# Kernel tuning notes

Hardware: AMD Instinct MI355X
Metric: run time of the kernel (lower is better)

## Reference

```python
import jax, jax.numpy as jnp
import numpy as np

N_STEPS = 8


def _step(state, qop, dz_sub, W1, b1, W2, b2, W3, b3, W4, b4):
    # state [B,4], qop [B,1], dz_sub [B,1] -> residual-updated state [B,4]
    inp = jnp.concatenate([state, qop, dz_sub], axis=-1)  # [B,6]
    h = jax.nn.silu(inp @ W1 + b1)
    h = jax.nn.silu(h @ W2 + b2)
    h = jax.nn.silu(h @ W3 + b3)
    return state + (h @ W4 + b4)


def setup_inputs() -> dict:
    key = jax.random.key(0)
    ks = jax.random.split(key, 8)
    B = 262144
    H = 256
    # scale weights like xavier-ish init so activations stay sane
    def w(k, shape):
        fan_in = shape[0]
        return jax.random.normal(k, shape, dtype=jnp.float32) * (1.0 / np.sqrt(fan_in))
    state_dz = jax.random.normal(ks[0], (B, 6), dtype=jnp.float32)
    z_frac = jax.random.uniform(ks[1], (B,), dtype=jnp.float32)
    return {
        "state_dz": state_dz,
        "z_frac": z_frac,
        "W1": w(ks[2], (6, H)), "b1": jnp.zeros((H,), jnp.float32),
        "W2": w(ks[3], (H, H)), "b2": jnp.zeros((H,), jnp.float32),
        "W3": w(ks[4], (H, H)), "b3": jnp.zeros((H,), jnp.float32),
        "W4": w(ks[5], (H, 4)) * 0.1, "b4": jnp.zeros((4,), jnp.float32),
    }


def reference(state_dz, z_frac, W1, b1, W2, b2, W3, b3, W4, b4):
    # Faithful translation of CompositionalPINN.forward with z_frac of shape [B].
    # Torch uses max_steps = n_full.max().item() (host sync); running all N_STEPS
    # with the per-sample mask (n_full > step) yields identical math, since the
    # mask is 0 for step >= n_full.
    state = state_dz[:, :4]
    qop = state_dz[:, 4:5]
    dz_total = state_dz[:, 5:6]
    dz_sub = dz_total / N_STEPS

    continuous_steps = z_frac * N_STEPS            # [B]
    n_full = jnp.floor(continuous_steps)           # [B], kept float (compared vs step)
    frac_partial = continuous_steps - n_full       # [B]

    for step in range(N_STEPS):
        mask = (n_full > step).astype(state.dtype)[:, None]  # [B,1]
        new_state = _step(state, qop, dz_sub, W1, b1, W2, b2, W3, b3, W4, b4)
        state = mask * new_state + (1.0 - mask) * state

    dz_partial = frac_partial[:, None] * dz_sub
    has_partial = (frac_partial > 1e-6).astype(state.dtype)[:, None]
    partial_state = _step(state, qop, dz_partial, W1, b1, W2, b2, W3, b3, W4, b4)
    state = has_partial * partial_state + (1.0 - has_partial) * state
    return state
```

## Files before the change

kernel.cpp:

```cpp
#include <hip/hip_runtime.h>

typedef unsigned short u16;
typedef unsigned int u32;
typedef __attribute__((ext_vector_type(8))) short v8s;
typedef __attribute__((ext_vector_type(4))) float f32x4;

#define RPB 64
#define THREADS 256
#define NSB 512
#define W1F 0
#define W2F 8192
#define W3F 73728
#define W4F 139264
#define TOTW 143360
#define BH_OFF 286720
#define PERM_OFF 305152

#define MFMA(w, b, c) __builtin_amdgcn_mfma_f32_16x16x32_bf16((w), (b), (c), 0, 0, 0)

typedef __attribute__((address_space(1))) const unsigned int gu32;
typedef __attribute__((address_space(3))) unsigned int su32;
__device__ __forceinline__ void gld16(const u16* g, u16* l) {
  __builtin_amdgcn_global_load_lds((gu32*)g, (su32*)l, 16, 0, 0);
}

__device__ __forceinline__ u32 pk2(float a, float b) {
  u32 r;
  asm("v_cvt_pk_bf16_f32 %0, %1, %2" : "=v"(r) : "v"(a), "v"(b));
  return r;
}
__device__ __forceinline__ float bfu(u32 w, int hi) {
  return __uint_as_float(hi ? (w & 0xffff0000u) : (w << 16));
}
__device__ __forceinline__ f32x4 silu4(f32x4 v) {
  f32x4 r;
#pragma unroll
  for (int i = 0; i < 4; ++i) r[i] = v[i] * __builtin_amdgcn_rcpf(1.0f + __expf(-v[i]));
  return r;
}

__global__ void prep_weights(const float* __restrict__ W1, const float* __restrict__ b1,
                             const float* __restrict__ W2, const float* __restrict__ W3,
                             const float* __restrict__ W4, u16* __restrict__ Wf) {
  int e = blockIdx.x * 256 + threadIdx.x;
  if (e >= TOTW) return;
  float val = 0.0f;
  if (e < W2F) {
    int mt = e >> 9, idx = e & 511, l = idx >> 3, j = idx & 7;
    int q = l >> 4, m = l & 15;
    int f = 16 * (j >> 2) + 4 * q + (j & 3);
    int col = mt * 16 + m;
    val = (f < 6) ? W1[f * 256 + col]
        : ((f < 12) ? W1[(f - 6) * 256 + col]
        : ((f == 12) ? b1[col] : 0.0f));
  } else if (e < W3F) {
    int e2 = e - W2F, blk = e2 >> 9, idx = e2 & 511, l = idx >> 3, j = idx & 7;
    int ks = blk >> 4, mt = blk & 15, q = l >> 4, m = l & 15;
    int f = 32 * ks + 16 * (j >> 2) + 4 * q + (j & 3);
    val = W2[f * 256 + mt * 16 + m];
  } else if (e < W4F) {
    int e2 = e - W3F, blk = e2 >> 9, idx = e2 & 511, l = idx >> 3, j = idx & 7;
    int ks = blk >> 4, mt = blk & 15, q = l >> 4, m = l & 15;
    int f = 32 * ks + 16 * (j >> 2) + 4 * q + (j & 3);
    val = W3[f * 256 + mt * 16 + m];
  } else {
    int e2 = e - W4F, ks = e2 >> 9, idx = e2 & 511, l = idx >> 3, j = idx & 7;
    int q = l >> 4, m = l & 15;
    int f = 32 * ks + 16 * (j >> 2) + 4 * q + (j & 3);
    val = (m < 4) ? W4[f * 4 + m] : 0.0f;
  }
  Wf[e] = (u16)pk2(val, val);
}

__global__ void hist_blocks(const float* __restrict__ zf, int* __restrict__ bh, int B) {
  __shared__ int h[9];
  int t = threadIdx.x;
  if (t < 9) h[t] = 0;
  __syncthreads();
  int r = blockIdx.x * 512 + t;
  if (r < B) {
    int nf = min(max((int)floorf(zf[r] * 8.0f), 0), 8);
    atomicAdd(&h[nf], 1);
  }
  __syncthreads();
  if (t < 9) bh[blockIdx.x * 9 + t] = h[t];
}

__global__ void scan_offsets(int* __restrict__ bh) {
  __shared__ int S[NSB * 9];
  __shared__ int tot[9], ebase[9];
  int t = threadIdx.x;
  for (int i = t; i < NSB * 9; i += 512) S[i] = bh[i];
  __syncthreads();
  if (t < 9) {
    int s = 0;
    for (int b = 0; b < NSB; ++b) s += S[b * 9 + t];
    tot[t] = s;
  }
  __syncthreads();
  if (t == 0) {
    int s = 0;
    for (int i = 0; i < 9; ++i) { ebase[i] = s; s += tot[i]; }
  }
  __syncthreads();
  if (t < 9) {
    int off = ebase[t];
    for (int b = 0; b < NSB; ++b) { int c = S[b * 9 + t]; S[b * 9 + t] = off; off += c; }
  }
  __syncthreads();
  for (int i = t; i < NSB * 9; i += 512) bh[i] = S[i];
}

__global__ void scatter_sorted(const float* __restrict__ zf, const int* __restrict__ bh,
                               int* __restrict__ perm, int B) {
  __shared__ int off[9];
  int t = threadIdx.x;
  if (t < 9) off[t] = bh[blockIdx.x * 9 + t];
  __syncthreads();
  int r = blockIdx.x * 512 + t;
  if (r < B) {
    int nf = min(max((int)floorf(zf[r] * 8.0f), 0), 8);
    int pos = atomicAdd(&off[nf], 1);
    perm[pos] = r;
  }
}

__global__ __attribute__((amdgpu_flat_work_group_size(256, 256)))
__attribute__((amdgpu_waves_per_eu(2, 2))) void pinn_main(
    const float* __restrict__ sdz, const float* __restrict__ zf,
    const u16* __restrict__ Wf, const int* __restrict__ perm,
    const float* __restrict__ b2, const float* __restrict__ b3,
    const float* __restrict__ b4, float* __restrict__ out) {
  __shared__ __align__(16) u16 ringS[3][8192];
  __shared__ __align__(16) u16 W1s[8192];
  __shared__ __align__(16) u16 W4s[4096];
  __shared__ __align__(16) float biasS[528];
  __shared__ __align__(16) float stS[RPB * 4];
  __shared__ float qopS[RPB], dzS[RPB], fracS[RPB];
  __shared__ int nfS[RPB], rowG[RPB];

  const int t = threadIdx.x;
  const int lane = t & 63;
  const int q = lane >> 4;
  const int n = lane & 15;
  const int wv = t >> 6;
  const int rb = wv * 16;

  if (t < RPB) {
    int rg = perm[blockIdx.x * RPB + t];
    rowG[t] = rg;
    const float* p = sdz + (size_t)rg * 6;
    stS[t * 4 + 0] = p[0]; stS[t * 4 + 1] = p[1];
    stS[t * 4 + 2] = p[2]; stS[t * 4 + 3] = p[3];
    qopS[t] = p[4];
    dzS[t] = p[5] * 0.125f;
    float cs = zf[rg] * 8.0f;
    float nfl = floorf(cs);
    nfS[t] = (int)nfl;
    fracS[t] = cs - nfl;
  }
  biasS[t] = b2[t]; biasS[256 + t] = b3[t];
  if (t < 16) biasS[512 + t] = (t < 4) ? b4[t] : 0.0f;
#pragma unroll
  for (int c = 0; c < 4; ++c)
    gld16(Wf + W1F + (c * 4 + wv) * 512 + lane * 8, &W1s[(c * 4 + wv) * 512]);
#pragma unroll
  for (int c = 0; c < 2; ++c)
    gld16(Wf + W4F + (c * 4 + wv) * 512 + lane * 8, &W4s[(c * 4 + wv) * 512]);
  __syncthreads();
  const int maxnf = nfS[RPB - 1];

  f32x4 acc[16];
  v8s bact[8];
  const f32x4 Z4 = {0.0f, 0.0f, 0.0f, 0.0f};

#define ISSUE_SLICE(AP, BUF)                                                  \
  do {                                                                        \
    int sp_ = (AP) & 15;                                                      \
    int off_ = ((sp_ >> 3) ? W3F : W2F) + (sp_ & 7) * 8192;                   \
    u16* dst_ = &ringS[(BUF)][0];                                             \
    _Pragma("unroll") for (int c_ = 0; c_ < 4; ++c_)                          \
      gld16(Wf + off_ + (c_ * 4 + wv) * 512 + lane * 8,                       \
            dst_ + (c_ * 4 + wv) * 512);                                      \
  } while (0)

  int ap = 0;
  int bc = 0;
  ISSUE_SLICE(0, 0);

#define PACK_BACT()                                              \
  do {                                                           \
    _Pragma("unroll") for (int ks = 0; ks < 8; ++ks) {           \
      f32x4 a0 = silu4(acc[2 * ks]);                             \
      f32x4 a1 = silu4(acc[2 * ks + 1]);                         \
      union { int4 i; v8s s; } u_;                               \
      u_.i.x = (int)pk2(a0[0], a0[1]);                           \
      u_.i.y = (int)pk2(a0[2], a0[3]);                           \
      u_.i.z = (int)pk2(a1[0], a1[1]);                           \
      u_.i.w = (int)pk2(a1[2], a1[3]);                           \
      bact[ks] = u_.s;                                           \
    }                                                            \
  } while (0)

  for (int ev = 0; ev <= maxnf; ++ev) {
    const bool partial = (ev == maxnf);

    v8s b1f;
    {
      const int row = rb + n;
      const float4 st = *(const float4*)&stS[row * 4];
      const float qop = qopS[row];
      const float dzv = partial ? fracS[row] * dzS[row] : dzS[row];
      u32 h01 = pk2(st.x, st.y), h23 = pk2(st.z, st.w), hqd = pk2(qop, dzv);
      float l0 = st.x - bfu(h01, 0), l1 = st.y - bfu(h01, 1);
      float l2 = st.z - bfu(h23, 0), l3 = st.w - bfu(h23, 1);
      float lq = qop - bfu(hqd, 0), ld = dzv - bfu(hqd, 1);
      u32 w0 = 0, w1 = 0;
      if (q == 0) { w0 = h01; w1 = h23; }
      else if (q == 1) { w0 = hqd; w1 = pk2(l0, l1); }
      else if (q == 2) { w0 = pk2(l2, l3); w1 = pk2(lq, ld); }
      else { w0 = 0x00003F80u; }
      union { int4 i; v8s s; } u_;
      u_.i.x = (int)w0; u_.i.y = (int)w1; u_.i.z = 0; u_.i.w = 0;
      b1f = u_.s;
    }

#pragma unroll
    for (int mt = 0; mt < 16; ++mt) {
      const v8s w = *(const v8s*)&W1s[mt * 512 + lane * 8];
      acc[mt] = MFMA(w, b1f, Z4);
    }
    PACK_BACT();

#pragma unroll
    for (int layer = 0; layer < 2; ++layer) {
      const int Lb = (layer == 0) ? 0 : 256;
#pragma unroll
      for (int mt = 0; mt < 16; ++mt) {
        const float4 bb = *(const float4*)&biasS[Lb + mt * 16 + q * 4];
        const f32x4 binit = {bb.x, bb.y, bb.z, bb.w};
        acc[mt] = binit;
      }
#pragma unroll
      for (int ks = 0; ks < 8; ++ks) {
        int bn = bc + 1; if (bn == 3) bn = 0;
        ISSUE_SLICE(ap + 1, bn);
        asm volatile("s_waitcnt vmcnt(4)" ::: "memory");
        __builtin_amdgcn_sched_barrier(0);
        __builtin_amdgcn_s_barrier();
        __builtin_amdgcn_sched_barrier(0);
        asm volatile("" ::: "memory");
        const u16* buf = &ringS[bc][0];
        __builtin_amdgcn_s_setprio(1);
#pragma unroll
        for (int i = 0; i < 8; ++i) {
          const v8s w = *(const v8s*)&buf[i * 512 + lane * 8];
          acc[i] = MFMA(w, bact[ks], acc[i]);
        }
        __builtin_amdgcn_sched_barrier(0);
#pragma unroll
        for (int i = 8; i < 16; ++i) {
          const v8s w = *(const v8s*)&buf[i * 512 + lane * 8];
          acc[i] = MFMA(w, bact[ks], acc[i]);
        }
        __builtin_amdgcn_s_setprio(0);
        bc = bn; ++ap;
      }
      PACK_BACT();
    }

    {
      const float4 bb = *(const float4*)&biasS[512 + q * 4];
      f32x4 a4 = {bb.x, bb.y, bb.z, bb.w};
#pragma unroll
      for (int ks = 0; ks < 8; ++ks) {
        const v8s w = *(const v8s*)&W4s[ks * 512 + lane * 8];
        a4 = MFMA(w, bact[ks], a4);
      }
      if (q == 0) {
        const int row = rb + n;
        const bool act = partial ? (fracS[row] > 1e-6f) : (nfS[row] > ev);
        if (act) {
          float4 cur = *(float4*)&stS[row * 4];
          cur.x += a4[0]; cur.y += a4[1];
          cur.z += a4[2]; cur.w += a4[3];
          *(float4*)&stS[row * 4] = cur;
        }
      }
    }
  }
  __syncthreads();

  {
    const int i = t;
    out[(size_t)rowG[i >> 2] * 4 + (i & 3)] = stS[i];
  }
}

extern "C" void kernel_launch(void* const* d_in, const int* in_sizes, int n_in,
                              void* d_out, int out_size, void* d_ws, size_t ws_size,
                              hipStream_t stream) {
  const float* sdz = (const float*)d_in[0];
  const float* zfr = (const float*)d_in[1];
  const float* W1 = (const float*)d_in[2];
  const float* b1 = (const float*)d_in[3];
  const float* W2 = (const float*)d_in[4];
  const float* b2 = (const float*)d_in[5];
  const float* W3 = (const float*)d_in[6];
  const float* b3 = (const float*)d_in[7];
  const float* W4 = (const float*)d_in[8];
  const float* b4 = (const float*)d_in[9];

  char* ws = (char*)d_ws;
  u16* Wf = (u16*)ws;
  int* bh = (int*)(ws + BH_OFF);
  int* perm = (int*)(ws + PERM_OFF);

  const int B = in_sizes[1];

  prep_weights<<<(TOTW + 255) / 256, 256, 0, stream>>>(W1, b1, W2, W3, W4, Wf);
  hist_blocks<<<NSB, 512, 0, stream>>>(zfr, bh, B);
  scan_offsets<<<1, 512, 0, stream>>>(bh);
  scatter_sorted<<<NSB, 512, 0, stream>>>(zfr, bh, perm, B);
  pinn_main<<<B / RPB, THREADS, 0, stream>>>(sdz, zfr, Wf, perm, b2, b3, b4,
                                             (float*)d_out);
}
```

Before: 526.6 us.

## Stream W1 and W4 through the LDS ring to cut shared memory, raise occupancy

Drops the dedicated W1 and W4 shared-memory buffers and streams those weights through the existing triple-buffered ring alongside the W2/W3 slices. Each evaluation becomes one continuous W1→W2→W3→W4 pipeline. Per-row metadata is also compacted: nf and has_partial go into one u16, dz*frac is precomputed, and rowG is re-read from perm at the end. Less LDS per block plus waves_per_eu raised to 3 lets more blocks fit per CU. The cost is extra barriers and global reloads of W1/W4 on every step, with possible register pressure at the higher occupancy target.

```diff
diff --git a/kernel.cpp b/kernel.cpp
--- a/kernel.cpp
+++ b/kernel.cpp
@@ -126,18 +126,16 @@
 }
 
 __global__ __attribute__((amdgpu_flat_work_group_size(256, 256)))
-__attribute__((amdgpu_waves_per_eu(2, 2))) void pinn_main(
+__attribute__((amdgpu_waves_per_eu(2, 3))) void pinn_main(
     const float* __restrict__ sdz, const float* __restrict__ zf,
     const u16* __restrict__ Wf, const int* __restrict__ perm,
     const float* __restrict__ b2, const float* __restrict__ b3,
     const float* __restrict__ b4, float* __restrict__ out) {
   __shared__ __align__(16) u16 ringS[3][8192];
-  __shared__ __align__(16) u16 W1s[8192];
-  __shared__ __align__(16) u16 W4s[4096];
   __shared__ __align__(16) float biasS[528];
   __shared__ __align__(16) float stS[RPB * 4];
-  __shared__ float qopS[RPB], dzS[RPB], fracS[RPB];
-  __shared__ int nfS[RPB], rowG[RPB];
+  __shared__ float qopS[RPB], dzS[RPB], dzpS[RPB];
+  __shared__ u16 nfS[RPB];
 
   const int t = threadIdx.x;
   const int lane = t & 63;
@@ -148,45 +146,57 @@
 
   if (t < RPB) {
     int rg = perm[blockIdx.x * RPB + t];
-    rowG[t] = rg;
     const float* p = sdz + (size_t)rg * 6;
     stS[t * 4 + 0] = p[0]; stS[t * 4 + 1] = p[1];
     stS[t * 4 + 2] = p[2]; stS[t * 4 + 3] = p[3];
     qopS[t] = p[4];
-    dzS[t] = p[5] * 0.125f;
+    float dzsub = p[5] * 0.125f;
+    dzS[t] = dzsub;
     float cs = zf[rg] * 8.0f;
     float nfl = floorf(cs);
-    nfS[t] = (int)nfl;
-    fracS[t] = cs - nfl;
+    float fr = cs - nfl;
+    dzpS[t] = fr * dzsub;
+    nfS[t] = (u16)((int)nfl | ((fr > 1e-6f) ? 256 : 0));
   }
   biasS[t] = b2[t]; biasS[256 + t] = b3[t];
   if (t < 16) biasS[512 + t] = (t < 4) ? b4[t] : 0.0f;
-#pragma unroll
-  for (int c = 0; c < 4; ++c)
-    gld16(Wf + W1F + (c * 4 + wv) * 512 + lane * 8, &W1s[(c * 4 + wv) * 512]);
-#pragma unroll
-  for (int c = 0; c < 2; ++c)
-    gld16(Wf + W4F + (c * 4 + wv) * 512 + lane * 8, &W4s[(c * 4 + wv) * 512]);
-  __syncthreads();
-  const int maxnf = nfS[RPB - 1];
+
+#define ISSUE16(OFF, BUF)                                                     \
+  do {                                                                        \
+    u16* dst_ = &ringS[(BUF)][0];                                             \
+    _Pragma("unroll") for (int c_ = 0; c_ < 4; ++c_)                          \
+      gld16(Wf + (OFF) + (c_ * 4 + wv) * 512 + lane * 8,                      \
+            dst_ + (c_ * 4 + wv) * 512);                                      \
+  } while (0)
+#define ISSUE8(OFF, BUF)                                                      \
+  do {                                                                        \
+    u16* dst_ = &ringS[(BUF)][0];                                             \
+    _Pragma("unroll") for (int c_ = 0; c_ < 2; ++c_)                          \
+      gld16(Wf + (OFF) + (c_ * 4 + wv) * 512 + lane * 8,                      \
+            dst_ + (c_ * 4 + wv) * 512);                                      \
+  } while (0)
+
+#define PHASE_SYNC4()                                                         \
+  asm volatile("s_waitcnt vmcnt(4)" ::: "memory");                            \
+  __builtin_amdgcn_sched_barrier(0);                                          \
+  __builtin_amdgcn_s_barrier();                                               \
+  __builtin_amdgcn_sched_barrier(0);                                          \
+  asm volatile("" ::: "memory");
+#define PHASE_SYNC2()                                                         \
+  asm volatile("s_waitcnt vmcnt(2)" ::: "memory");                            \
+  __builtin_amdgcn_sched_barrier(0);                                          \
+  __builtin_amdgcn_s_barrier();                                               \
+  __builtin_amdgcn_sched_barrier(0);                                          \
+  asm volatile("" ::: "memory");
+
+  ISSUE16(W1F, 0);
+  __syncthreads();
+  const int maxnf = nfS[RPB - 1] & 255;
+  int bc = 0;
 
   f32x4 acc[16];
   v8s bact[8];
   const f32x4 Z4 = {0.0f, 0.0f, 0.0f, 0.0f};
-
-#define ISSUE_SLICE(AP, BUF)                                                  \
-  do {                                                                        \
-    int sp_ = (AP) & 15;                                                      \
-    int off_ = ((sp_ >> 3) ? W3F : W2F) + (sp_ & 7) * 8192;                   \
-    u16* dst_ = &ringS[(BUF)][0];                                             \
-    _Pragma("unroll") for (int c_ = 0; c_ < 4; ++c_)                          \
-      gld16(Wf + off_ + (c_ * 4 + wv) * 512 + lane * 8,                       \
-            dst_ + (c_ * 4 + wv) * 512);                                      \
-  } while (0)
-
-  int ap = 0;
-  int bc = 0;
-  ISSUE_SLICE(0, 0);
 
 #define PACK_BACT()                                              \
   do {                                                           \
@@ -210,7 +220,7 @@
       const int row = rb + n;
       const float4 st = *(const float4*)&stS[row * 4];
       const float qop = qopS[row];
-      const float dzv = partial ? fracS[row] * dzS[row] : dzS[row];
+      const float dzv = partial ? dzpS[row] : dzS[row];
       u32 h01 = pk2(st.x, st.y), h23 = pk2(st.z, st.w), hqd = pk2(qop, dzv);
       float l0 = st.x - bfu(h01, 0), l1 = st.y - bfu(h01, 1);
       float l2 = st.z - bfu(h23, 0), l3 = st.w - bfu(h23, 1);
@@ -225,10 +235,25 @@
       b1f = u_.s;
     }
 
-#pragma unroll
-    for (int mt = 0; mt < 16; ++mt) {
-      const v8s w = *(const v8s*)&W1s[mt * 512 + lane * 8];
-      acc[mt] = MFMA(w, b1f, Z4);
+    {
+      int bn = bc + 1; if (bn == 3) bn = 0;
+      ISSUE16(W2F, bn);
+      PHASE_SYNC4();
+      const u16* buf = &ringS[bc][0];
+      __builtin_amdgcn_s_setprio(1);
+#pragma unroll
+      for (int mt = 0; mt < 8; ++mt) {
+        const v8s w = *(const v8s*)&buf[mt * 512 + lane * 8];
+        acc[mt] = MFMA(w, b1f, Z4);
+      }
+      __builtin_amdgcn_sched_barrier(0);
+#pragma unroll
+      for (int mt = 8; mt < 16; ++mt) {
+        const v8s w = *(const v8s*)&buf[mt * 512 + lane * 8];
+        acc[mt] = MFMA(w, b1f, Z4);
+      }
+      __builtin_amdgcn_s_setprio(0);
+      bc = bn;
     }
     PACK_BACT();
 
@@ -242,44 +267,54 @@
         acc[mt] = binit;
       }
 #pragma unroll
-      for (int ks = 0; ks < 8; ++ks) {
+      for (int ph = 0; ph < 8; ++ph) {
         int bn = bc + 1; if (bn == 3) bn = 0;
-        ISSUE_SLICE(ap + 1, bn);
-        asm volatile("s_waitcnt vmcnt(4)" ::: "memory");
-        __builtin_amdgcn_sched_barrier(0);
-        __builtin_amdgcn_s_barrier();
-        __builtin_amdgcn_sched_barrier(0);
-        asm volatile("" ::: "memory");
+        if (layer == 1 && ph == 7) {
+          ISSUE8(W4F, bn);
+          PHASE_SYNC2();
+        } else {
+          const int noff = (ph < 7) ? ((layer ? W3F : W2F) + (ph + 1) * 8192)
+                                    : W3F;
+          ISSUE16(noff, bn);
+          PHASE_SYNC4();
+        }
         const u16* buf = &ringS[bc][0];
         __builtin_amdgcn_s_setprio(1);
 #pragma unroll
         for (int i = 0; i < 8; ++i) {
           const v8s w = *(const v8s*)&buf[i * 512 + lane * 8];
-          acc[i] = MFMA(w, bact[ks], acc[i]);
+          acc[i] = MFMA(w, bact[ph], acc[i]);
         }
         __builtin_amdgcn_sched_barrier(0);
 #pragma unroll
         for (int i = 8; i < 16; ++i) {
           const v8s w = *(const v8s*)&buf[i * 512 + lane * 8];
-          acc[i] = MFMA(w, bact[ks], acc[i]);
+          acc[i] = MFMA(w, bact[ph], acc[i]);
         }
         __builtin_amdgcn_s_setprio(0);
-        bc = bn; ++ap;
+        bc = bn;
       }
       PACK_BACT();
     }
 
     {
+      int bn = bc + 1; if (bn == 3) bn = 0;
+      ISSUE16(W1F, bn);
+      PHASE_SYNC4();
+      const u16* buf = &ringS[bc][0];
       const float4 bb = *(const float4*)&biasS[512 + q * 4];
       f32x4 a4 = {bb.x, bb.y, bb.z, bb.w};
+      __builtin_amdgcn_s_setprio(1);
 #pragma unroll
       for (int ks = 0; ks < 8; ++ks) {
-        const v8s w = *(const v8s*)&W4s[ks * 512 + lane * 8];
+        const v8s w = *(const v8s*)&buf[ks * 512 + lane * 8];
         a4 = MFMA(w, bact[ks], a4);
       }
+      __builtin_amdgcn_s_setprio(0);
       if (q == 0) {
         const int row = rb + n;
-        const bool act = partial ? (fracS[row] > 1e-6f) : (nfS[row] > ev);
+        const u16 nfv = nfS[row];
+        const bool act = partial ? (nfv >> 8) : ((nfv & 255) > ev);
         if (act) {
           float4 cur = *(float4*)&stS[row * 4];
           cur.x += a4[0]; cur.y += a4[1];
@@ -287,13 +322,14 @@
           *(float4*)&stS[row * 4] = cur;
         }
       }
+      bc = bn;
     }
   }
   __syncthreads();
 
   {
-    const int i = t;
-    out[(size_t)rowG[i >> 2] * 4 + (i & 3)] = stS[i];
+    int r = perm[blockIdx.x * RPB + (t >> 2)];
+    out[(size_t)r * 4 + (t & 3)] = stS[t];
   }
 }
 
```

Result: slower. 553.0 us (+5.0%).

## Process two 16-row tiles per wave to reuse streamed weight slices

Applied to the files above, without the earlier changes.

Doubles the rows per block from 64 to 128, with each wave computing two 16-row N tiles. Every W1/W2/W3/W4 fragment read from LDS now feeds two MFMAs instead of one. The goal is to halve the weight streaming from global into the LDS ring, and the per-MFMA LDS reads, per row processed. The cost is roughly double the accumulator and activation registers, with occupancy relaxed to allow one wave per EU, and fewer blocks overall. Separately, the partial-step dz value and the has-partial flag are precomputed into LDS, with the flag packed into the nf word.

```diff
diff --git a/kernel.cpp b/kernel.cpp
--- a/kernel.cpp
+++ b/kernel.cpp
@@ -5,7 +5,7 @@
 typedef __attribute__((ext_vector_type(8))) short v8s;
 typedef __attribute__((ext_vector_type(4))) float f32x4;
 
-#define RPB 64
+#define RPB 128
 #define THREADS 256
 #define NSB 512
 #define W1F 0
@@ -126,7 +126,7 @@
 }
 
 __global__ __attribute__((amdgpu_flat_work_group_size(256, 256)))
-__attribute__((amdgpu_waves_per_eu(2, 2))) void pinn_main(
+__attribute__((amdgpu_waves_per_eu(1, 2))) void pinn_main(
     const float* __restrict__ sdz, const float* __restrict__ zf,
     const u16* __restrict__ Wf, const int* __restrict__ perm,
     const float* __restrict__ b2, const float* __restrict__ b3,
@@ -136,7 +136,7 @@
   __shared__ __align__(16) u16 W4s[4096];
   __shared__ __align__(16) float biasS[528];
   __shared__ __align__(16) float stS[RPB * 4];
-  __shared__ float qopS[RPB], dzS[RPB], fracS[RPB];
+  __shared__ float qopS[RPB], dzS[RPB], dzpS[RPB];
   __shared__ int nfS[RPB], rowG[RPB];
 
   const int t = threadIdx.x;
@@ -144,7 +144,7 @@
   const int q = lane >> 4;
   const int n = lane & 15;
   const int wv = t >> 6;
-  const int rb = wv * 16;
+  const int rb = wv * 32;
 
   if (t < RPB) {
     int rg = perm[blockIdx.x * RPB + t];
@@ -153,11 +153,13 @@
     stS[t * 4 + 0] = p[0]; stS[t * 4 + 1] = p[1];
     stS[t * 4 + 2] = p[2]; stS[t * 4 + 3] = p[3];
     qopS[t] = p[4];
-    dzS[t] = p[5] * 0.125f;
+    float dzsub = p[5] * 0.125f;
+    dzS[t] = dzsub;
     float cs = zf[rg] * 8.0f;
     float nfl = floorf(cs);
-    nfS[t] = (int)nfl;
-    fracS[t] = cs - nfl;
+    float fr = cs - nfl;
+    dzpS[t] = fr * dzsub;
+    nfS[t] = (int)nfl | ((fr > 1e-6f) ? 256 : 0);
   }
   biasS[t] = b2[t]; biasS[256 + t] = b3[t];
   if (t < 16) biasS[512 + t] = (t < 4) ? b4[t] : 0.0f;
@@ -168,10 +170,10 @@
   for (int c = 0; c < 2; ++c)
     gld16(Wf + W4F + (c * 4 + wv) * 512 + lane * 8, &W4s[(c * 4 + wv) * 512]);
   __syncthreads();
-  const int maxnf = nfS[RPB - 1];
-
-  f32x4 acc[16];
-  v8s bact[8];
+  const int maxnf = nfS[RPB - 1] & 255;
+
+  f32x4 acc[16][2];
+  v8s bact[8][2];
   const f32x4 Z4 = {0.0f, 0.0f, 0.0f, 0.0f};
 
 #define ISSUE_SLICE(AP, BUF)                                                  \
@@ -191,26 +193,29 @@
 #define PACK_BACT()                                              \
   do {                                                           \
     _Pragma("unroll") for (int ks = 0; ks < 8; ++ks) {           \
-      f32x4 a0 = silu4(acc[2 * ks]);                             \
-      f32x4 a1 = silu4(acc[2 * ks + 1]);                         \
-      union { int4 i; v8s s; } u_;                               \
-      u_.i.x = (int)pk2(a0[0], a0[1]);                           \
-      u_.i.y = (int)pk2(a0[2], a0[3]);                           \
-      u_.i.z = (int)pk2(a1[0], a1[1]);                           \
-      u_.i.w = (int)pk2(a1[2], a1[3]);                           \
-      bact[ks] = u_.s;                                           \
+      _Pragma("unroll") for (int nt = 0; nt < 2; ++nt) {         \
+        f32x4 a0 = silu4(acc[2 * ks][nt]);                       \
+        f32x4 a1 = silu4(acc[2 * ks + 1][nt]);                   \
+        union { int4 i; v8s s; } u_;                             \
+        u_.i.x = (int)pk2(a0[0], a0[1]);                         \
+        u_.i.y = (int)pk2(a0[2], a0[3]);                         \
+        u_.i.z = (int)pk2(a1[0], a1[1]);                         \
+        u_.i.w = (int)pk2(a1[2], a1[3]);                         \
+        bact[ks][nt] = u_.s;                                     \
+      }                                                          \
     }                                                            \
   } while (0)
 
   for (int ev = 0; ev <= maxnf; ++ev) {
     const bool partial = (ev == maxnf);
 
-    v8s b1f;
-    {
-      const int row = rb + n;
+    v8s b1f[2];
+#pragma unroll
+    for (int nt = 0; nt < 2; ++nt) {
+      const int row = rb + nt * 16 + n;
       const float4 st = *(const float4*)&stS[row * 4];
       const float qop = qopS[row];
-      const float dzv = partial ? fracS[row] * dzS[row] : dzS[row];
+      const float dzv = partial ? dzpS[row] : dzS[row];
       u32 h01 = pk2(st.x, st.y), h23 = pk2(st.z, st.w), hqd = pk2(qop, dzv);
       float l0 = st.x - bfu(h01, 0), l1 = st.y - bfu(h01, 1);
       float l2 = st.z - bfu(h23, 0), l3 = st.w - bfu(h23, 1);
@@ -222,13 +227,19 @@
       else { w0 = 0x00003F80u; }
       union { int4 i; v8s s; } u_;
       u_.i.x = (int)w0; u_.i.y = (int)w1; u_.i.z = 0; u_.i.w = 0;
-      b1f = u_.s;
+      b1f[nt] = u_.s;
     }
 
 #pragma unroll
-    for (int mt = 0; mt < 16; ++mt) {
-      const v8s w = *(const v8s*)&W1s[mt * 512 + lane * 8];
-      acc[mt] = MFMA(w, b1f, Z4);
+    for (int grp = 0; grp < 4; ++grp) {
+#pragma unroll
+      for (int i2 = 0; i2 < 4; ++i2) {
+        const int mt = grp * 4 + i2;
+        const v8s w = *(const v8s*)&W1s[mt * 512 + lane * 8];
+        acc[mt][0] = MFMA(w, b1f[0], Z4);
+        acc[mt][1] = MFMA(w, b1f[1], Z4);
+      }
+      __builtin_amdgcn_sched_barrier(0);
     }
     PACK_BACT();
 
@@ -239,7 +250,8 @@
       for (int mt = 0; mt < 16; ++mt) {
         const float4 bb = *(const float4*)&biasS[Lb + mt * 16 + q * 4];
         const f32x4 binit = {bb.x, bb.y, bb.z, bb.w};
-        acc[mt] = binit;
+        acc[mt][0] = binit;
+        acc[mt][1] = binit;
       }
 #pragma unroll
       for (int ks = 0; ks < 8; ++ks) {
@@ -253,15 +265,15 @@
         const u16* buf = &ringS[bc][0];
         __builtin_amdgcn_s_setprio(1);
 #pragma unroll
-        for (int i = 0; i < 8; ++i) {
-          const v8s w = *(const v8s*)&buf[i * 512 + lane * 8];
-          acc[i] = MFMA(w, bact[ks], acc[i]);
-        }
-        __builtin_amdgcn_sched_barrier(0);
-#pragma unroll
-        for (int i = 8; i < 16; ++i) {
-          const v8s w = *(const v8s*)&buf[i * 512 + lane * 8];
-          acc[i] = MFMA(w, bact[ks], acc[i]);
+        for (int grp = 0; grp < 4; ++grp) {
+#pragma unroll
+          for (int i2 = 0; i2 < 4; ++i2) {
+            const int i = grp * 4 + i2;
+            const v8s w = *(const v8s*)&buf[i * 512 + lane * 8];
+            acc[i][0] = MFMA(w, bact[ks][0], acc[i][0]);
+            acc[i][1] = MFMA(w, bact[ks][1], acc[i][1]);
+          }
+          __builtin_amdgcn_sched_barrier(0);
         }
         __builtin_amdgcn_s_setprio(0);
         bc = bn; ++ap;
@@ -271,30 +283,37 @@
 
     {
       const float4 bb = *(const float4*)&biasS[512 + q * 4];
-      f32x4 a4 = {bb.x, bb.y, bb.z, bb.w};
+      f32x4 a4[2];
+      a4[0] = (f32x4){bb.x, bb.y, bb.z, bb.w};
+      a4[1] = a4[0];
 #pragma unroll
       for (int ks = 0; ks < 8; ++ks) {
         const v8s w = *(const v8s*)&W4s[ks * 512 + lane * 8];
-        a4 = MFMA(w, bact[ks], a4);
+        a4[0] = MFMA(w, bact[ks][0], a4[0]);
+        a4[1] = MFMA(w, bact[ks][1], a4[1]);
+        if ((ks & 3) == 3) __builtin_amdgcn_sched_barrier(0);
       }
       if (q == 0) {
-        const int row = rb + n;
-        const bool act = partial ? (fracS[row] > 1e-6f) : (nfS[row] > ev);
-        if (act) {
-          float4 cur = *(float4*)&stS[row * 4];
-          cur.x += a4[0]; cur.y += a4[1];
-          cur.z += a4[2]; cur.w += a4[3];
-          *(float4*)&stS[row * 4] = cur;
+#pragma unroll
+        for (int nt = 0; nt < 2; ++nt) {
+          const int row = rb + nt * 16 + n;
+          const int nfv = nfS[row];
+          const bool act = partial ? (nfv >> 8) : ((nfv & 255) > ev);
+          if (act) {
+            float4 cur = *(float4*)&stS[row * 4];
+            cur.x += a4[nt][0]; cur.y += a4[nt][1];
+            cur.z += a4[nt][2]; cur.w += a4[nt][3];
+            *(float4*)&stS[row * 4] = cur;
+          }
         }
       }
     }
   }
   __syncthreads();
 
-  {
-    const int i = t;
+#pragma unroll
+  for (int i = t; i < RPB * 4; i += THREADS)
     out[(size_t)rowG[i >> 2] * 4 + (i & 3)] = stS[i];
-  }
 }
 
 extern "C" void kernel_launch(void* const* d_in, const int* in_sizes, int n_in,
```

Result: slower. 690.9 us (+31.2%).

## Split weight slices between LDS ring and direct-to-register global loads

Applied to the files above, without the earlier changes.

Each 16-tile weight slice for layers 2 and 3 is now split: 12 tiles still stream through the LDS ring buffer, and the last 4 tiles are loaded straight from global memory into double-buffered registers. This shrinks the LDS ring and cuts LDS read traffic per MFMA step. The waves-per-EU hint is relaxed to allow more registers, and extra sched barriers group the MFMAs. The costs are higher VGPR pressure, possible loss of occupancy, and more global-load latency exposed on the critical path, which now waits on a deeper vmcnt.

```diff
diff --git a/kernel.cpp b/kernel.cpp
--- a/kernel.cpp
+++ b/kernel.cpp
@@ -126,12 +126,12 @@
 }
 
 __global__ __attribute__((amdgpu_flat_work_group_size(256, 256)))
-__attribute__((amdgpu_waves_per_eu(2, 2))) void pinn_main(
+__attribute__((amdgpu_waves_per_eu(1, 2))) void pinn_main(
     const float* __restrict__ sdz, const float* __restrict__ zf,
     const u16* __restrict__ Wf, const int* __restrict__ perm,
     const float* __restrict__ b2, const float* __restrict__ b3,
     const float* __restrict__ b4, float* __restrict__ out) {
-  __shared__ __align__(16) u16 ringS[3][8192];
+  __shared__ __align__(16) u16 ringS[3][6144];
   __shared__ __align__(16) u16 W1s[8192];
   __shared__ __align__(16) u16 W4s[4096];
   __shared__ __align__(16) float biasS[528];
@@ -167,26 +167,24 @@
 #pragma unroll
   for (int c = 0; c < 2; ++c)
     gld16(Wf + W4F + (c * 4 + wv) * 512 + lane * 8, &W4s[(c * 4 + wv) * 512]);
-  __syncthreads();
-  const int maxnf = nfS[RPB - 1];
 
   f32x4 acc[16];
   v8s bact[8];
+  v8s wreg[2][4];
   const f32x4 Z4 = {0.0f, 0.0f, 0.0f, 0.0f};
 
-#define ISSUE_SLICE(AP, BUF)                                                  \
-  do {                                                                        \
-    int sp_ = (AP) & 15;                                                      \
-    int off_ = ((sp_ >> 3) ? W3F : W2F) + (sp_ & 7) * 8192;                   \
-    u16* dst_ = &ringS[(BUF)][0];                                             \
-    _Pragma("unroll") for (int c_ = 0; c_ < 4; ++c_)                          \
-      gld16(Wf + off_ + (c_ * 4 + wv) * 512 + lane * 8,                       \
-            dst_ + (c_ * 4 + wv) * 512);                                      \
-  } while (0)
-
-  int ap = 0;
+  {
+    u16* dst_ = &ringS[0][0];
+#pragma unroll
+    for (int c_ = 0; c_ < 3; ++c_)
+      gld16(Wf + W2F + (c_ * 4 + wv) * 512 + lane * 8, dst_ + (c_ * 4 + wv) * 512);
+    const v8s* gsrc = (const v8s*)(Wf + W2F);
+#pragma unroll
+    for (int j = 0; j < 4; ++j) wreg[0][j] = gsrc[(12 + j) * 64 + lane];
+  }
+  __syncthreads();
+  const int maxnf = nfS[RPB - 1];
   int bc = 0;
-  ISSUE_SLICE(0, 0);
 
 #define PACK_BACT()                                              \
   do {                                                           \
@@ -229,6 +227,7 @@
     for (int mt = 0; mt < 16; ++mt) {
       const v8s w = *(const v8s*)&W1s[mt * 512 + lane * 8];
       acc[mt] = MFMA(w, b1f, Z4);
+      if ((mt & 3) == 3) __builtin_amdgcn_sched_barrier(0);
     }
     PACK_BACT();
 
@@ -243,9 +242,26 @@
       }
 #pragma unroll
       for (int ks = 0; ks < 8; ++ks) {
+        const int pc = ((layer << 3) + ks) & 1;
         int bn = bc + 1; if (bn == 3) bn = 0;
-        ISSUE_SLICE(ap + 1, bn);
-        asm volatile("s_waitcnt vmcnt(4)" ::: "memory");
+        {
+          const int sp = ((layer << 3) + ks + 1) & 15;
+          const int noff = ((sp >> 3) ? W3F : W2F) + (sp & 7) * 8192;
+          u16* dst_ = &ringS[bn][0];
+#pragma unroll
+          for (int c_ = 0; c_ < 3; ++c_)
+            gld16(Wf + noff + (c_ * 4 + wv) * 512 + lane * 8,
+                  dst_ + (c_ * 4 + wv) * 512);
+          const v8s* gsrc = (const v8s*)(Wf + noff);
+          if (pc == 0) {
+#pragma unroll
+            for (int j = 0; j < 4; ++j) wreg[1][j] = gsrc[(12 + j) * 64 + lane];
+          } else {
+#pragma unroll
+            for (int j = 0; j < 4; ++j) wreg[0][j] = gsrc[(12 + j) * 64 + lane];
+          }
+        }
+        asm volatile("s_waitcnt vmcnt(7)" ::: "memory");
         __builtin_amdgcn_sched_barrier(0);
         __builtin_amdgcn_s_barrier();
         __builtin_amdgcn_sched_barrier(0);
@@ -253,18 +269,26 @@
         const u16* buf = &ringS[bc][0];
         __builtin_amdgcn_s_setprio(1);
 #pragma unroll
-        for (int i = 0; i < 8; ++i) {
-          const v8s w = *(const v8s*)&buf[i * 512 + lane * 8];
-          acc[i] = MFMA(w, bact[ks], acc[i]);
+        for (int grp = 0; grp < 3; ++grp) {
+#pragma unroll
+          for (int i2 = 0; i2 < 4; ++i2) {
+            const int i = grp * 4 + i2;
+            const v8s w = *(const v8s*)&buf[i * 512 + lane * 8];
+            acc[i] = MFMA(w, bact[ks], acc[i]);
+          }
+          __builtin_amdgcn_sched_barrier(0);
         }
-        __builtin_amdgcn_sched_barrier(0);
-#pragma unroll
-        for (int i = 8; i < 16; ++i) {
-          const v8s w = *(const v8s*)&buf[i * 512 + lane * 8];
-          acc[i] = MFMA(w, bact[ks], acc[i]);
+        if (pc == 0) {
+#pragma unroll
+          for (int j = 0; j < 4; ++j)
+            acc[12 + j] = MFMA(wreg[0][j], bact[ks], acc[12 + j]);
+        } else {
+#pragma unroll
+          for (int j = 0; j < 4; ++j)
+            acc[12 + j] = MFMA(wreg[1][j], bact[ks], acc[12 + j]);
         }
         __builtin_amdgcn_s_setprio(0);
-        bc = bn; ++ap;
+        bc = bn;
       }
       PACK_BACT();
     }
@@ -276,6 +300,7 @@
       for (int ks = 0; ks < 8; ++ks) {
         const v8s w = *(const v8s*)&W4s[ks * 512 + lane * 8];
         a4 = MFMA(w, bact[ks], a4);
+        if ((ks & 3) == 3) __builtin_amdgcn_sched_barrier(0);
       }
       if (q == 0) {
         const int row = rb + n;
```

Measured after the change: 1.081 ms. 2.05x slower.
